# Optimization experiments

Hardware: AMD Instinct MI355X
Metric: run time of the kernel (lower is better)

The kernel has to match this reference:

```python
import jax, jax.numpy as jnp
import numpy as np

N = 100000   # num nodes
F = 256      # feat_data dim == args.feat_dim (required by concat shapes)
D = 32       # fixed neighbor count per node
B = 8192     # batch of node indices
NEG = 10     # neg_sample_size (hard-coded in module)


def setup_inputs() -> dict:
    key = jax.random.key(0)
    ks = jax.random.split(key, 9)
    feat_data = jax.random.normal(ks[0], (N, F), dtype=jnp.float32)
    # self.feats[i] = [degrees[i]] * feat_dim
    degrees = jax.random.randint(ks[1], (N,), 1, 64).astype(jnp.float32)
    feats = jnp.tile(degrees[:, None], (1, F))
    W1 = jax.random.normal(ks[2], (F, 2 * F), dtype=jnp.float32) * 0.02
    b1 = jnp.zeros((F,), dtype=jnp.float32)
    W2 = jax.random.normal(ks[3], (F, 2 * F), dtype=jnp.float32) * 0.02
    b2 = jnp.zeros((F,), dtype=jnp.float32)
    adj = jax.random.randint(ks[4], (N, D), 0, N)          # adj_lists as fixed-degree matrix
    inputs1 = jax.random.randint(ks[5], (B,), 0, N)
    inputs2 = jax.random.randint(ks[6], (B,), 0, N)
    neg = jax.random.randint(ks[7], (NEG,), 0, N)           # unigram neg samples (passed in for determinism)
    return dict(feat_data=feat_data, feats=feats, W1=W1, b1=b1, W2=W2, b2=b2,
                adj=adj, inputs1=inputs1, inputs2=inputs2, neg=neg)


def _aggregate(feat_data, feats, W1, b1, W2, b2, adj, nodes):
    # aggregator(nodes): for each node, agg_one_hop over its neighbors, summed.
    node_feats = feat_data[nodes]                            # [B, F]
    nb = adj[nodes]                                          # [B, D]
    # agg_one_hop: linear1(concat(feat_data[nb], feats[nb]))
    nb_in = jnp.concatenate([feat_data[nb], feats[nb]], axis=-1)   # [B, D, 2F]
    emb = jnp.einsum('bdk,ok->bdo', nb_in, W1) + b1          # [B, D, F]
    neighbor_emb = emb.sum(axis=1)                           # [B, F] (bias summed D times, as in torch)
    final_in = jnp.concatenate([node_feats, neighbor_emb], axis=-1)  # [B, 2F]
    return final_in @ W2.T + b2                              # [B, F]


def _l2norm(x):
    # F.normalize(x, dim=1), eps=1e-12
    n = jnp.linalg.norm(x, axis=1, keepdims=True)
    return x / jnp.maximum(n, 1e-12)


def reference(feat_data, feats, W1, b1, W2, b2, adj, inputs1, inputs2, neg):
    out1 = _l2norm(_aggregate(feat_data, feats, W1, b1, W2, b2, adj, inputs1))
    out2 = _l2norm(_aggregate(feat_data, feats, W1, b1, W2, b2, adj, inputs2))
    neg_out = _l2norm(_aggregate(feat_data, feats, W1, b1, W2, b2, adj, neg))
    return (out1, out2, neg_out)
```

## Files before the change

### kernel.cpp

```cpp
#include <hip/hip_runtime.h>
#include <hip/hip_bf16.h>
#include <hip/hip_fp8.h>

#define FDIM 256
#define K2   512
#define DNB  32
#define TM   32
#define NMAX 100000
#define TMAX 20480
#define CONVB 2048

typedef __attribute__((ext_vector_type(8))) short bf16x8;
typedef __attribute__((ext_vector_type(4))) float f32x4;
typedef __attribute__((ext_vector_type(2))) float f32x2;
typedef __attribute__((ext_vector_type(4))) unsigned int u32x4;
typedef __attribute__((ext_vector_type(2))) unsigned int u32x2;

__device__ __align__(16) unsigned char g_FDb[(size_t)NMAX * FDIM];
__device__ __align__(16) unsigned short g_Xb[(size_t)TMAX * K2];
__device__ float g_degb[NMAX];
__device__ float g_Sdegb[TMAX];
__device__ __align__(16) unsigned short g_Wc[FDIM * K2];
__device__ float g_c2[FDIM];
__device__ float g_c3[FDIM];

__device__ __forceinline__ unsigned short f2bf(float f) {
    __hip_bfloat16 h = __float2bfloat16(f);
    return *reinterpret_cast<unsigned short*>(&h);
}

__device__ __forceinline__ unsigned int enc4(float a, float b, float c, float d) {
#if __has_builtin(__builtin_amdgcn_cvt_pk_fp8_f32)
    int w = 0;
    w = __builtin_amdgcn_cvt_pk_fp8_f32(a, b, w, false);
    w = __builtin_amdgcn_cvt_pk_fp8_f32(c, d, w, true);
    return (unsigned int)w;
#else
    __hip_fp8_e4m3 ha(a), hb(b), hc(c), hd(d);
    return (unsigned)ha.__x | ((unsigned)hb.__x << 8) |
           ((unsigned)hc.__x << 16) | ((unsigned)hd.__x << 24);
#endif
}
__device__ __forceinline__ f32x4 dec4(unsigned int w) {
#if __has_builtin(__builtin_amdgcn_cvt_pk_f32_fp8)
    f32x2 lo = __builtin_amdgcn_cvt_pk_f32_fp8((int)w, false);
    f32x2 hi = __builtin_amdgcn_cvt_pk_f32_fp8((int)w, true);
    return (f32x4){lo.x, lo.y, hi.x, hi.y};
#else
    __hip_fp8_e4m3 h0, h1, h2, h3;
    h0.__x = (unsigned char)(w);
    h1.__x = (unsigned char)(w >> 8);
    h2.__x = (unsigned char)(w >> 16);
    h3.__x = (unsigned char)(w >> 24);
    return (f32x4){(float)h0, (float)h1, (float)h2, (float)h3};
#endif
}

__global__ __launch_bounds__(256) void build_prep(
    const float* __restrict__ fd,
    const float* __restrict__ feats,
    const float* __restrict__ W1,
    const float* __restrict__ W2,
    const float* __restrict__ b1,
    const float* __restrict__ b2,
    float Dmul, int N,
    unsigned char* tab_p, float* deg_p)
{
    unsigned char* tab = tab_p ? tab_p : g_FDb;
    float* deg = deg_p ? deg_p : g_degb;
    int bid = blockIdx.x;
    int tid = threadIdx.x;

    if (bid >= 256) {
        size_t tidg = (size_t)(bid - 256) * 256 + tid;
        size_t nthr = (size_t)CONVB * 256;
        size_t total16 = (size_t)N * (FDIM / 16);
        const f32x4* in4 = (const f32x4*)fd;
        u32x4* out16 = (u32x4*)tab;

        size_t i = tidg;
        for (; i + nthr < total16; i += 2 * nthr) {
            f32x4 a0 = __builtin_nontemporal_load(in4 + 4 * i);
            f32x4 a1 = __builtin_nontemporal_load(in4 + 4 * i + 1);
            f32x4 a2 = __builtin_nontemporal_load(in4 + 4 * i + 2);
            f32x4 a3 = __builtin_nontemporal_load(in4 + 4 * i + 3);
            size_t j = i + nthr;
            f32x4 b0 = __builtin_nontemporal_load(in4 + 4 * j);
            f32x4 b1v = __builtin_nontemporal_load(in4 + 4 * j + 1);
            f32x4 b2v = __builtin_nontemporal_load(in4 + 4 * j + 2);
            f32x4 b3 = __builtin_nontemporal_load(in4 + 4 * j + 3);
            u32x4 oa, ob;
            oa.x = enc4(a0.x, a0.y, a0.z, a0.w);
            oa.y = enc4(a1.x, a1.y, a1.z, a1.w);
            oa.z = enc4(a2.x, a2.y, a2.z, a2.w);
            oa.w = enc4(a3.x, a3.y, a3.z, a3.w);
            ob.x = enc4(b0.x, b0.y, b0.z, b0.w);
            ob.y = enc4(b1v.x, b1v.y, b1v.z, b1v.w);
            ob.z = enc4(b2v.x, b2v.y, b2v.z, b2v.w);
            ob.w = enc4(b3.x, b3.y, b3.z, b3.w);
            out16[i] = oa;
            out16[j] = ob;
        }
        for (; i < total16; i += nthr) {
            f32x4 a0 = __builtin_nontemporal_load(in4 + 4 * i);
            f32x4 a1 = __builtin_nontemporal_load(in4 + 4 * i + 1);
            f32x4 a2 = __builtin_nontemporal_load(in4 + 4 * i + 2);
            f32x4 a3 = __builtin_nontemporal_load(in4 + 4 * i + 3);
            u32x4 o;
            o.x = enc4(a0.x, a0.y, a0.z, a0.w);
            o.y = enc4(a1.x, a1.y, a1.z, a1.w);
            o.z = enc4(a2.x, a2.y, a2.z, a2.w);
            o.w = enc4(a3.x, a3.y, a3.z, a3.w);
            out16[i] = o;
        }
        return;
    }

    __shared__ float w2s[FDIM];
    __shared__ float rv[4], ru[4];
    int o = bid;

    for (size_t n = (size_t)o * 256 + tid; n < (size_t)N; n += 65536)
        deg[n] = feats[n * FDIM];

    w2s[tid] = W2[(size_t)o * K2 + FDIM + tid];
    __syncthreads();

    const float* w1a = W1 + tid;
    const float* w1b = W1 + FDIM + tid;
    float acc0 = 0.f, acc1 = 0.f;
    for (int j = 0; j < FDIM; j += 8) {
        float r0[8], r1[8];
        #pragma unroll
        for (int u = 0; u < 8; ++u) {
            r0[u] = w1a[(size_t)(j + u) * K2];
            r1[u] = w1b[(size_t)(j + u) * K2];
        }
        #pragma unroll
        for (int u = 0; u < 8; ++u) {
            acc0 = fmaf(w2s[j + u], r0[u], acc0);
            acc1 = fmaf(w2s[j + u], r1[u], acc1);
        }
    }
    g_Wc[(size_t)o * K2 + FDIM + tid] = f2bf(acc0);
    g_Wc[(size_t)o * K2 + tid]        = f2bf(W2[(size_t)o * K2 + tid]);

    float v = acc1;
    float u = b1[tid] * w2s[tid];
    #pragma unroll
    for (int s = 32; s; s >>= 1) { v += __shfl_down(v, s); u += __shfl_down(u, s); }
    if ((tid & 63) == 0) { rv[tid >> 6] = v; ru[tid >> 6] = u; }
    __syncthreads();
    if (tid == 0) {
        g_c2[o] = rv[0] + rv[1] + rv[2] + rv[3];
        g_c3[o] = b2[o] + Dmul * (ru[0] + ru[1] + ru[2] + ru[3]);
    }
}

__global__ __launch_bounds__(256, 8) void gather(
    const unsigned char* tab_p, const float* deg_p,
    const int* __restrict__ adj,
    const int* __restrict__ in1, int B1,
    const int* __restrict__ in2, int B2,
    const int* __restrict__ neg, int total,
    unsigned short* X_p, float* Sdeg_p)
{
    const unsigned char* tab = tab_p ? tab_p : g_FDb;
    const float* deg = deg_p ? deg_p : g_degb;
    unsigned short* X = X_p ? X_p : g_Xb;
    float* Sdeg = Sdeg_p ? Sdeg_p : g_Sdegb;

    int wave = threadIdx.x >> 6, lane = threadIdx.x & 63;
    int half = lane >> 5, l31 = lane & 31;
    int t = blockIdx.x * 4 + wave;
    if (t >= total) return;
    int node = (t < B1) ? in1[t] : ((t < B1 + B2) ? in2[t - B1] : neg[t - B1 - B2]);

    int idx = 0; float dg = 0.f;
    if (lane < DNB) {
        idx = adj[(size_t)node * DNB + lane];
        dg = deg[idx];
    }
    #pragma unroll
    for (int s = 16; s; s >>= 1) dg += __shfl_down(dg, s);
    if (lane == 0) Sdeg[t] = dg;

    unsigned int nw = *(const unsigned int*)(tab + (size_t)node * FDIM + lane * 4);
    f32x4 nf = dec4(nw);
    *(ushort4*)(X + (size_t)t * K2 + lane * 4) =
        make_ushort4(f2bf(nf.x), f2bf(nf.y), f2bf(nf.z), f2bf(nf.w));

    float acc[8];
    #pragma unroll
    for (int k = 0; k < 8; ++k) acc[k] = 0.f;
    #pragma unroll
    for (int d = 0; d < DNB; d += 16) {
        u32x2 v[8];
        #pragma unroll
        for (int u = 0; u < 8; ++u) {
            int nb = __shfl(idx, d + u * 2 + half);
            v[u] = *(const u32x2*)(tab + (size_t)nb * FDIM + l31 * 8);
        }
        #pragma unroll
        for (int u = 0; u < 8; ++u) {
            f32x4 lo = dec4(v[u].x);
            f32x4 hi = dec4(v[u].y);
            acc[0] += lo.x; acc[1] += lo.y; acc[2] += lo.z; acc[3] += lo.w;
            acc[4] += hi.x; acc[5] += hi.y; acc[6] += hi.z; acc[7] += hi.w;
        }
    }
    #pragma unroll
    for (int k = 0; k < 8; ++k) acc[k] += __shfl_xor(acc[k], 32);

    if (lane < 32) {
        bf16x8 ah;
        #pragma unroll
        for (int k = 0; k < 8; ++k) ah[k] = (short)f2bf(acc[k]);
        *(bf16x8*)(X + (size_t)t * K2 + FDIM + l31 * 8) = ah;
    }
}

__global__ __launch_bounds__(256, 4) void gemm_norm(const unsigned short* X_p,
                                                    const float* Sdeg_p,
                                                    float* __restrict__ out, int total)
{
    const unsigned short* X = X_p ? X_p : g_Xb;
    const float* SdegG = Sdeg_p ? Sdeg_p : g_Sdegb;

    __shared__ __align__(16) char lds[TM * 1024];
    __shared__ float Sdeg[TM];

    int tid = threadIdx.x, wave = tid >> 6, lane = tid & 63;
    int base = blockIdx.x * TM;

    if (tid < TM) {
        int t = base + tid;
        Sdeg[tid] = (t < total) ? SdegG[t] : 0.f;
    }
    #pragma unroll
    for (int i = 0; i < 8; ++i) {
        int row = wave * 8 + i;
        int t = base + row;
        bf16x8 v = {0, 0, 0, 0, 0, 0, 0, 0};
        if (t < total) v = *(const bf16x8*)(X + (size_t)t * K2 + lane * 8);
        *(bf16x8*)(lds + row * 1024 + ((lane * 16) ^ ((row & 7) << 4))) = v;
    }
    __syncthreads();

    int l15 = lane & 15, lg = lane >> 4;
    int swzA = (l15 & 7) << 4;
    f32x4 acc[2][4];
    #pragma unroll
    for (int mt = 0; mt < 2; ++mt)
        #pragma unroll
        for (int nt = 0; nt < 4; ++nt) acc[mt][nt] = (f32x4){0.f, 0.f, 0.f, 0.f};

    const char* pA0 = lds + (size_t)l15 * 1024;
    const char* pA1 = lds + (size_t)(16 + l15) * 1024;
    const unsigned short* wcB = g_Wc + (size_t)(wave * 64 + l15) * K2 + lg * 8;

    #pragma unroll 4
    for (int kk = 0; kk < K2; kk += 32) {
        int kb = kk * 2 + lg * 16;
        bf16x8 a0 = *(const bf16x8*)(pA0 + (kb ^ swzA));
        bf16x8 a1 = *(const bf16x8*)(pA1 + (kb ^ swzA));
        #pragma unroll
        for (int nt = 0; nt < 4; ++nt) {
            bf16x8 b = *(const bf16x8*)(wcB + (size_t)nt * 16 * K2 + kk);
            acc[0][nt] = __builtin_amdgcn_mfma_f32_16x16x32_bf16(a0, b, acc[0][nt], 0, 0, 0);
            acc[1][nt] = __builtin_amdgcn_mfma_f32_16x16x32_bf16(a1, b, acc[1][nt], 0, 0, 0);
        }
    }
    __syncthreads();

    float* outf = (float*)lds;
    #pragma unroll
    for (int mt = 0; mt < 2; ++mt)
        #pragma unroll
        for (int nt = 0; nt < 4; ++nt)
            #pragma unroll
            for (int r = 0; r < 4; ++r) {
                int row = mt * 16 + lg * 4 + r;
                int col = wave * 64 + nt * 16 + l15;
                outf[row * 256 + col] = acc[mt][nt][r];
            }
    __syncthreads();

    float4 c2v = *(const float4*)(g_c2 + lane * 4);
    float4 c3v = *(const float4*)(g_c3 + lane * 4);
    for (int r = 0; r < 8; ++r) {
        int row = wave * 8 + r;
        int t = base + row;
        if (t >= total) break;
        float sd = Sdeg[row];
        float4 v = *(float4*)(outf + row * 256 + lane * 4);
        v.x += sd * c2v.x + c3v.x;
        v.y += sd * c2v.y + c3v.y;
        v.z += sd * c2v.z + c3v.z;
        v.w += sd * c2v.w + c3v.w;
        float ss = v.x * v.x + v.y * v.y + v.z * v.z + v.w * v.w;
        #pragma unroll
        for (int s = 32; s; s >>= 1) ss += __shfl_xor(ss, s);
        float inv = 1.0f / fmaxf(sqrtf(ss), 1e-12f);
        f32x4 o;
        o.x = v.x * inv; o.y = v.y * inv; o.z = v.z * inv; o.w = v.w * inv;
        __builtin_nontemporal_store(o, (f32x4*)(out + (size_t)t * FDIM + lane * 4));
    }
}

extern "C" void kernel_launch(void* const* d_in, const int* in_sizes, int n_in,
                              void* d_out, int out_size, void* d_ws, size_t ws_size,
                              hipStream_t stream) {
    const float* feat_data = (const float*)d_in[0];
    const float* feats     = (const float*)d_in[1];
    const float* W1        = (const float*)d_in[2];
    const float* b1        = (const float*)d_in[3];
    const float* W2        = (const float*)d_in[4];
    const float* b2        = (const float*)d_in[5];
    const int*   adj       = (const int*)d_in[6];
    const int*   in1       = (const int*)d_in[7];
    const int*   in2       = (const int*)d_in[8];
    const int*   neg       = (const int*)d_in[9];

    int B1 = in_sizes[7];
    int B2 = in_sizes[8];
    int Bn = in_sizes[9];
    int N  = in_sizes[0] / FDIM;
    int D  = in_sizes[6] / N;

    float* out = (float*)d_out;
    int total = B1 + B2 + Bn;

    size_t off = 0;
    auto take = [&](size_t bytes) { size_t o = off; off = (off + bytes + 255) & ~(size_t)255; return o; };
    size_t tab_o  = take((size_t)N * FDIM);
    size_t x_o    = take((size_t)total * K2 * 2);
    size_t deg_o  = take((size_t)N * 4);
    size_t sdeg_o = take((size_t)total * 4);
    bool usews = (ws_size >= off);

    char* wsb = (char*)d_ws;
    unsigned char* tab  = usews ? (unsigned char*)(wsb + tab_o) : nullptr;
    unsigned short* X   = usews ? (unsigned short*)(wsb + x_o)  : nullptr;
    float* deg  = usews ? (float*)(wsb + deg_o)  : nullptr;
    float* Sdeg = usews ? (float*)(wsb + sdeg_o) : nullptr;

    build_prep<<<256 + CONVB, 256, 0, stream>>>(feat_data, feats, W1, W2, b1, b2,
                                                (float)D, N, tab, deg);
    gather<<<(total + 3) / 4, 256, 0, stream>>>(tab, deg, adj, in1, B1, in2, B2,
                                                neg, total, X, Sdeg);
    gemm_norm<<<(total + TM - 1) / TM, 256, 0, stream>>>(X, Sdeg, out, total);
}
```

Measured before the change: 100.6 us.

## Fuse neighbor gather into GEMM+normalize kernel, dropping intermediate X buffer

Merges the gather kernel and the gemm_norm kernel into one 512-thread kernel. Each wave gathers 4 rows of node and summed-neighbor features straight into swizzled LDS, then every wave runs MFMA on a 16-row by 64-column tile. This removes the global round trip of the bf16 X matrix and the Sdeg array, and saves one kernel launch. In exchange the gather and the GEMM no longer overlap across kernels, and each block now holds its LDS through the latency-bound gather phase, which may lower occupancy.

```diff
diff --git a/kernel.cpp b/kernel.cpp
--- a/kernel.cpp
+++ b/kernel.cpp
@@ -7,7 +7,6 @@
 #define DNB  32
 #define TM   32
 #define NMAX 100000
-#define TMAX 20480
 #define CONVB 2048
 
 typedef __attribute__((ext_vector_type(8))) short bf16x8;
@@ -17,9 +16,7 @@
 typedef __attribute__((ext_vector_type(2))) unsigned int u32x2;
 
 __device__ __align__(16) unsigned char g_FDb[(size_t)NMAX * FDIM];
-__device__ __align__(16) unsigned short g_Xb[(size_t)TMAX * K2];
 __device__ float g_degb[NMAX];
-__device__ float g_Sdegb[TMAX];
 __device__ __align__(16) unsigned short g_Wc[FDIM * K2];
 __device__ float g_c2[FDIM];
 __device__ float g_c3[FDIM];
@@ -157,139 +154,126 @@
     }
 }
 
-__global__ __launch_bounds__(256, 8) void gather(
+__global__ __launch_bounds__(512, 4) void gg_norm(
     const unsigned char* tab_p, const float* deg_p,
     const int* __restrict__ adj,
     const int* __restrict__ in1, int B1,
     const int* __restrict__ in2, int B2,
     const int* __restrict__ neg, int total,
-    unsigned short* X_p, float* Sdeg_p)
+    float* __restrict__ out)
 {
     const unsigned char* tab = tab_p ? tab_p : g_FDb;
     const float* deg = deg_p ? deg_p : g_degb;
-    unsigned short* X = X_p ? X_p : g_Xb;
-    float* Sdeg = Sdeg_p ? Sdeg_p : g_Sdegb;
-
-    int wave = threadIdx.x >> 6, lane = threadIdx.x & 63;
-    int half = lane >> 5, l31 = lane & 31;
-    int t = blockIdx.x * 4 + wave;
-    if (t >= total) return;
-    int node = (t < B1) ? in1[t] : ((t < B1 + B2) ? in2[t - B1] : neg[t - B1 - B2]);
-
-    int idx = 0; float dg = 0.f;
-    if (lane < DNB) {
-        idx = adj[(size_t)node * DNB + lane];
-        dg = deg[idx];
-    }
-    #pragma unroll
-    for (int s = 16; s; s >>= 1) dg += __shfl_down(dg, s);
-    if (lane == 0) Sdeg[t] = dg;
-
-    unsigned int nw = *(const unsigned int*)(tab + (size_t)node * FDIM + lane * 4);
-    f32x4 nf = dec4(nw);
-    *(ushort4*)(X + (size_t)t * K2 + lane * 4) =
-        make_ushort4(f2bf(nf.x), f2bf(nf.y), f2bf(nf.z), f2bf(nf.w));
-
-    float acc[8];
-    #pragma unroll
-    for (int k = 0; k < 8; ++k) acc[k] = 0.f;
-    #pragma unroll
-    for (int d = 0; d < DNB; d += 16) {
-        u32x2 v[8];
-        #pragma unroll
-        for (int u = 0; u < 8; ++u) {
-            int nb = __shfl(idx, d + u * 2 + half);
-            v[u] = *(const u32x2*)(tab + (size_t)nb * FDIM + l31 * 8);
-        }
-        #pragma unroll
-        for (int u = 0; u < 8; ++u) {
-            f32x4 lo = dec4(v[u].x);
-            f32x4 hi = dec4(v[u].y);
-            acc[0] += lo.x; acc[1] += lo.y; acc[2] += lo.z; acc[3] += lo.w;
-            acc[4] += hi.x; acc[5] += hi.y; acc[6] += hi.z; acc[7] += hi.w;
-        }
-    }
-    #pragma unroll
-    for (int k = 0; k < 8; ++k) acc[k] += __shfl_xor(acc[k], 32);
-
-    if (lane < 32) {
-        bf16x8 ah;
-        #pragma unroll
-        for (int k = 0; k < 8; ++k) ah[k] = (short)f2bf(acc[k]);
-        *(bf16x8*)(X + (size_t)t * K2 + FDIM + l31 * 8) = ah;
-    }
-}
-
-__global__ __launch_bounds__(256, 4) void gemm_norm(const unsigned short* X_p,
-                                                    const float* Sdeg_p,
-                                                    float* __restrict__ out, int total)
-{
-    const unsigned short* X = X_p ? X_p : g_Xb;
-    const float* SdegG = Sdeg_p ? Sdeg_p : g_Sdegb;
 
     __shared__ __align__(16) char lds[TM * 1024];
     __shared__ float Sdeg[TM];
 
     int tid = threadIdx.x, wave = tid >> 6, lane = tid & 63;
+    int half = lane >> 5, l31 = lane & 31;
     int base = blockIdx.x * TM;
 
-    if (tid < TM) {
-        int t = base + tid;
-        Sdeg[tid] = (t < total) ? SdegG[t] : 0.f;
-    }
-    #pragma unroll
-    for (int i = 0; i < 8; ++i) {
-        int row = wave * 8 + i;
+    #pragma unroll
+    for (int i = 0; i < 4; ++i) {
+        int row = wave * 4 + i;
         int t = base + row;
-        bf16x8 v = {0, 0, 0, 0, 0, 0, 0, 0};
-        if (t < total) v = *(const bf16x8*)(X + (size_t)t * K2 + lane * 8);
-        *(bf16x8*)(lds + row * 1024 + ((lane * 16) ^ ((row & 7) << 4))) = v;
+        char* rowp = lds + row * 1024;
+        int swz = (row & 7) << 4;
+        if (t >= total) {
+            ushort4 z4 = make_ushort4(0, 0, 0, 0);
+            *(ushort4*)(rowp + ((lane * 8) ^ swz)) = z4;
+            if (lane < 32) {
+                bf16x8 z8 = {0, 0, 0, 0, 0, 0, 0, 0};
+                *(bf16x8*)(rowp + 512 + ((l31 * 16) ^ swz)) = z8;
+            }
+            if (lane == 0) Sdeg[row] = 0.f;
+            continue;
+        }
+        int node = (t < B1) ? in1[t] : ((t < B1 + B2) ? in2[t - B1] : neg[t - B1 - B2]);
+
+        int idx = 0; float dg = 0.f;
+        if (lane < DNB) {
+            idx = adj[(size_t)node * DNB + lane];
+            dg = deg[idx];
+        }
+        #pragma unroll
+        for (int s = 16; s; s >>= 1) dg += __shfl_down(dg, s);
+        if (lane == 0) Sdeg[row] = dg;
+
+        unsigned int nw = *(const unsigned int*)(tab + (size_t)node * FDIM + lane * 4);
+        f32x4 nf = dec4(nw);
+        *(ushort4*)(rowp + ((lane * 8) ^ swz)) =
+            make_ushort4(f2bf(nf.x), f2bf(nf.y), f2bf(nf.z), f2bf(nf.w));
+
+        float acc[8];
+        #pragma unroll
+        for (int k = 0; k < 8; ++k) acc[k] = 0.f;
+        #pragma unroll
+        for (int d = 0; d < DNB; d += 16) {
+            u32x2 v[8];
+            #pragma unroll
+            for (int u = 0; u < 8; ++u) {
+                int nb = __shfl(idx, d + u * 2 + half);
+                v[u] = *(const u32x2*)(tab + (size_t)nb * FDIM + l31 * 8);
+            }
+            #pragma unroll
+            for (int u = 0; u < 8; ++u) {
+                f32x4 lo = dec4(v[u].x);
+                f32x4 hi = dec4(v[u].y);
+                acc[0] += lo.x; acc[1] += lo.y; acc[2] += lo.z; acc[3] += lo.w;
+                acc[4] += hi.x; acc[5] += hi.y; acc[6] += hi.z; acc[7] += hi.w;
+            }
+        }
+        #pragma unroll
+        for (int k = 0; k < 8; ++k) acc[k] += __shfl_xor(acc[k], 32);
+
+        if (lane < 32) {
+            bf16x8 ah;
+            #pragma unroll
+            for (int k = 0; k < 8; ++k) ah[k] = (short)f2bf(acc[k]);
+            *(bf16x8*)(rowp + 512 + ((l31 * 16) ^ swz)) = ah;
+        }
     }
     __syncthreads();
 
     int l15 = lane & 15, lg = lane >> 4;
     int swzA = (l15 & 7) << 4;
-    f32x4 acc[2][4];
-    #pragma unroll
-    for (int mt = 0; mt < 2; ++mt)
-        #pragma unroll
-        for (int nt = 0; nt < 4; ++nt) acc[mt][nt] = (f32x4){0.f, 0.f, 0.f, 0.f};
-
-    const char* pA0 = lds + (size_t)l15 * 1024;
-    const char* pA1 = lds + (size_t)(16 + l15) * 1024;
-    const unsigned short* wcB = g_Wc + (size_t)(wave * 64 + l15) * K2 + lg * 8;
+    int mt = wave >> 2;
+    int c0 = (wave & 3) * 64;
+    f32x4 acc[4];
+    #pragma unroll
+    for (int nt = 0; nt < 4; ++nt) acc[nt] = (f32x4){0.f, 0.f, 0.f, 0.f};
+
+    const char* pA = lds + (size_t)(mt * 16 + l15) * 1024;
+    const unsigned short* wcB = g_Wc + (size_t)(c0 + l15) * K2 + lg * 8;
 
     #pragma unroll 4
     for (int kk = 0; kk < K2; kk += 32) {
         int kb = kk * 2 + lg * 16;
-        bf16x8 a0 = *(const bf16x8*)(pA0 + (kb ^ swzA));
-        bf16x8 a1 = *(const bf16x8*)(pA1 + (kb ^ swzA));
+        bf16x8 a0 = *(const bf16x8*)(pA + (kb ^ swzA));
         #pragma unroll
         for (int nt = 0; nt < 4; ++nt) {
             bf16x8 b = *(const bf16x8*)(wcB + (size_t)nt * 16 * K2 + kk);
-            acc[0][nt] = __builtin_amdgcn_mfma_f32_16x16x32_bf16(a0, b, acc[0][nt], 0, 0, 0);
-            acc[1][nt] = __builtin_amdgcn_mfma_f32_16x16x32_bf16(a1, b, acc[1][nt], 0, 0, 0);
+            acc[nt] = __builtin_amdgcn_mfma_f32_16x16x32_bf16(a0, b, acc[nt], 0, 0, 0);
         }
     }
     __syncthreads();
 
     float* outf = (float*)lds;
     #pragma unroll
-    for (int mt = 0; mt < 2; ++mt)
-        #pragma unroll
-        for (int nt = 0; nt < 4; ++nt)
-            #pragma unroll
-            for (int r = 0; r < 4; ++r) {
-                int row = mt * 16 + lg * 4 + r;
-                int col = wave * 64 + nt * 16 + l15;
-                outf[row * 256 + col] = acc[mt][nt][r];
-            }
+    for (int nt = 0; nt < 4; ++nt)
+        #pragma unroll
+        for (int r = 0; r < 4; ++r) {
+            int row = mt * 16 + lg * 4 + r;
+            int col = c0 + nt * 16 + l15;
+            outf[row * 256 + col] = acc[nt][r];
+        }
     __syncthreads();
 
     float4 c2v = *(const float4*)(g_c2 + lane * 4);
     float4 c3v = *(const float4*)(g_c3 + lane * 4);
-    for (int r = 0; r < 8; ++r) {
-        int row = wave * 8 + r;
+    #pragma unroll
+    for (int r = 0; r < 4; ++r) {
+        int row = wave * 4 + r;
         int t = base + row;
         if (t >= total) break;
         float sd = Sdeg[row];
@@ -331,23 +315,14 @@
     float* out = (float*)d_out;
     int total = B1 + B2 + Bn;
 
-    size_t off = 0;
-    auto take = [&](size_t bytes) { size_t o = off; off = (off + bytes + 255) & ~(size_t)255; return o; };
-    size_t tab_o  = take((size_t)N * FDIM);
-    size_t x_o    = take((size_t)total * K2 * 2);
-    size_t deg_o  = take((size_t)N * 4);
-    size_t sdeg_o = take((size_t)total * 4);
-    bool usews = (ws_size >= off);
-
-    char* wsb = (char*)d_ws;
-    unsigned char* tab  = usews ? (unsigned char*)(wsb + tab_o) : nullptr;
-    unsigned short* X   = usews ? (unsigned short*)(wsb + x_o)  : nullptr;
-    float* deg  = usews ? (float*)(wsb + deg_o)  : nullptr;
-    float* Sdeg = usews ? (float*)(wsb + sdeg_o) : nullptr;
+    size_t tab_bytes = (size_t)N * FDIM;
+    size_t need = ((tab_bytes + 255) & ~(size_t)255) + (size_t)N * 4;
+    bool usews = (ws_size >= need);
+    unsigned char* tab = usews ? (unsigned char*)d_ws : nullptr;
+    float* deg = usews ? (float*)((char*)d_ws + ((tab_bytes + 255) & ~(size_t)255)) : nullptr;
 
     build_prep<<<256 + CONVB, 256, 0, stream>>>(feat_data, feats, W1, W2, b1, b2,
                                                 (float)D, N, tab, deg);
-    gather<<<(total + 3) / 4, 256, 0, stream>>>(tab, deg, adj, in1, B1, in2, B2,
-                                                neg, total, X, Sdeg);
-    gemm_norm<<<(total + TM - 1) / TM, 256, 0, stream>>>(X, Sdeg, out, total);
-}
+    gg_norm<<<(total + TM - 1) / TM, 512, 0, stream>>>(tab, deg, adj, in1, B1,
+                                                       in2, B2, neg, total, out);
+}
```

New measurement: 114.2 us. 1.14x slower.

## Store intermediate X in FP8 instead of BF16 and issue all neighbor loads upfront

Applied to the files above, without the earlier changes.

The intermediate activation buffer X written by gather and read by gemm_norm now holds FP8 bytes instead of BF16, halving its size. The node features are copied raw and the summed neighbor features are re-encoded to FP8, then gemm_norm decodes and converts to BF16 when staging into LDS. The neighbor loads are also merged into a single batch of 16 loads per lane to expose more memory parallelism. Quantizing the 32-neighbor sum to FP8 adds precision loss and extra conversion work in the GEMM prologue.

```diff
diff --git a/kernel.cpp b/kernel.cpp
--- a/kernel.cpp
+++ b/kernel.cpp
@@ -17,7 +17,7 @@
 typedef __attribute__((ext_vector_type(2))) unsigned int u32x2;
 
 __device__ __align__(16) unsigned char g_FDb[(size_t)NMAX * FDIM];
-__device__ __align__(16) unsigned short g_Xb[(size_t)TMAX * K2];
+__device__ __align__(16) unsigned char g_Xb[(size_t)TMAX * K2];
 __device__ float g_degb[NMAX];
 __device__ float g_Sdegb[TMAX];
 __device__ __align__(16) unsigned short g_Wc[FDIM * K2];
@@ -163,11 +163,11 @@
     const int* __restrict__ in1, int B1,
     const int* __restrict__ in2, int B2,
     const int* __restrict__ neg, int total,
-    unsigned short* X_p, float* Sdeg_p)
+    unsigned char* X_p, float* Sdeg_p)
 {
     const unsigned char* tab = tab_p ? tab_p : g_FDb;
     const float* deg = deg_p ? deg_p : g_degb;
-    unsigned short* X = X_p ? X_p : g_Xb;
+    unsigned char* X = X_p ? X_p : g_Xb;
     float* Sdeg = Sdeg_p ? Sdeg_p : g_Sdegb;
 
     int wave = threadIdx.x >> 6, lane = threadIdx.x & 63;
@@ -186,45 +186,40 @@
     if (lane == 0) Sdeg[t] = dg;
 
     unsigned int nw = *(const unsigned int*)(tab + (size_t)node * FDIM + lane * 4);
-    f32x4 nf = dec4(nw);
-    *(ushort4*)(X + (size_t)t * K2 + lane * 4) =
-        make_ushort4(f2bf(nf.x), f2bf(nf.y), f2bf(nf.z), f2bf(nf.w));
-
+    *(unsigned int*)(X + (size_t)t * K2 + lane * 4) = nw;
+
+    u32x2 v[16];
+    #pragma unroll
+    for (int u = 0; u < 16; ++u) {
+        int nb = __shfl(idx, u * 2 + half);
+        v[u] = *(const u32x2*)(tab + (size_t)nb * FDIM + l31 * 8);
+    }
     float acc[8];
     #pragma unroll
     for (int k = 0; k < 8; ++k) acc[k] = 0.f;
     #pragma unroll
-    for (int d = 0; d < DNB; d += 16) {
-        u32x2 v[8];
-        #pragma unroll
-        for (int u = 0; u < 8; ++u) {
-            int nb = __shfl(idx, d + u * 2 + half);
-            v[u] = *(const u32x2*)(tab + (size_t)nb * FDIM + l31 * 8);
-        }
-        #pragma unroll
-        for (int u = 0; u < 8; ++u) {
-            f32x4 lo = dec4(v[u].x);
-            f32x4 hi = dec4(v[u].y);
-            acc[0] += lo.x; acc[1] += lo.y; acc[2] += lo.z; acc[3] += lo.w;
-            acc[4] += hi.x; acc[5] += hi.y; acc[6] += hi.z; acc[7] += hi.w;
-        }
+    for (int u = 0; u < 16; ++u) {
+        f32x4 lo = dec4(v[u].x);
+        f32x4 hi = dec4(v[u].y);
+        acc[0] += lo.x; acc[1] += lo.y; acc[2] += lo.z; acc[3] += lo.w;
+        acc[4] += hi.x; acc[5] += hi.y; acc[6] += hi.z; acc[7] += hi.w;
     }
     #pragma unroll
     for (int k = 0; k < 8; ++k) acc[k] += __shfl_xor(acc[k], 32);
 
     if (lane < 32) {
-        bf16x8 ah;
-        #pragma unroll
-        for (int k = 0; k < 8; ++k) ah[k] = (short)f2bf(acc[k]);
-        *(bf16x8*)(X + (size_t)t * K2 + FDIM + l31 * 8) = ah;
-    }
-}
-
-__global__ __launch_bounds__(256, 4) void gemm_norm(const unsigned short* X_p,
+        u32x2 o;
+        o.x = enc4(acc[0], acc[1], acc[2], acc[3]);
+        o.y = enc4(acc[4], acc[5], acc[6], acc[7]);
+        *(u32x2*)(X + (size_t)t * K2 + FDIM + l31 * 8) = o;
+    }
+}
+
+__global__ __launch_bounds__(256, 4) void gemm_norm(const unsigned char* X_p,
                                                     const float* Sdeg_p,
                                                     float* __restrict__ out, int total)
 {
-    const unsigned short* X = X_p ? X_p : g_Xb;
+    const unsigned char* X = X_p ? X_p : g_Xb;
     const float* SdegG = Sdeg_p ? Sdeg_p : g_Sdegb;
 
     __shared__ __align__(16) char lds[TM * 1024];
@@ -241,9 +236,16 @@
     for (int i = 0; i < 8; ++i) {
         int row = wave * 8 + i;
         int t = base + row;
-        bf16x8 v = {0, 0, 0, 0, 0, 0, 0, 0};
-        if (t < total) v = *(const bf16x8*)(X + (size_t)t * K2 + lane * 8);
-        *(bf16x8*)(lds + row * 1024 + ((lane * 16) ^ ((row & 7) << 4))) = v;
+        u32x2 v = (u32x2){0u, 0u};
+        if (t < total) v = *(const u32x2*)(X + (size_t)t * K2 + lane * 8);
+        f32x4 lo = dec4(v.x);
+        f32x4 hi = dec4(v.y);
+        bf16x8 h;
+        h[0] = (short)f2bf(lo.x); h[1] = (short)f2bf(lo.y);
+        h[2] = (short)f2bf(lo.z); h[3] = (short)f2bf(lo.w);
+        h[4] = (short)f2bf(hi.x); h[5] = (short)f2bf(hi.y);
+        h[6] = (short)f2bf(hi.z); h[7] = (short)f2bf(hi.w);
+        *(bf16x8*)(lds + row * 1024 + ((lane * 16) ^ ((row & 7) << 4))) = h;
     }
     __syncthreads();
 
@@ -334,14 +336,14 @@
     size_t off = 0;
     auto take = [&](size_t bytes) { size_t o = off; off = (off + bytes + 255) & ~(size_t)255; return o; };
     size_t tab_o  = take((size_t)N * FDIM);
-    size_t x_o    = take((size_t)total * K2 * 2);
+    size_t x_o    = take((size_t)total * K2);
     size_t deg_o  = take((size_t)N * 4);
     size_t sdeg_o = take((size_t)total * 4);
     bool usews = (ws_size >= off);
 
     char* wsb = (char*)d_ws;
-    unsigned char* tab  = usews ? (unsigned char*)(wsb + tab_o) : nullptr;
-    unsigned short* X   = usews ? (unsigned short*)(wsb + x_o)  : nullptr;
+    unsigned char* tab = usews ? (unsigned char*)(wsb + tab_o) : nullptr;
+    unsigned char* X   = usews ? (unsigned char*)(wsb + x_o)   : nullptr;
     float* deg  = usews ? (float*)(wsb + deg_o)  : nullptr;
     float* Sdeg = usews ? (float*)(wsb + sdeg_o) : nullptr;
 
```

New measurement: 97.54 us. -3.1%, faster.
